# Kernel optimization log

Measured on AMD Instinct MI355X. Metric: run time of the kernel, lower is better.

Reference implementation:

```python
import jax, jax.numpy as jnp
import numpy as np

NUM_HEADS = 16

def _apply_rope(t, cos, sin):
    # t: [B, nh, S, hd]; cos/sin: [S, hd//2]
    t1 = t[..., 0::2]
    t2 = t[..., 1::2]
    c = cos[None, None, :, :]
    s = sin[None, None, :, :]
    r1 = t1 * c - t2 * s
    r2 = t1 * s + t2 * c
    # interleave back to [..., hd]
    out = jnp.stack([r1, r2], axis=-1)
    return out.reshape(t.shape)

def setup_inputs() -> dict:
    key = jax.random.key(0)
    ks = jax.random.split(key, 6)
    B, S, H = 1, 4096, 1024
    hd = H // NUM_HEADS
    x = jax.random.normal(ks[0], (B, S, H), dtype=jnp.float32)
    # RoPE angle matrix: theta[pos, i] = pos / 10000^(2i/hd), shape [context, hd//2]
    pos = jnp.arange(S, dtype=jnp.float32)[:, None]
    inv_freq = 1.0 / (10000.0 ** (jnp.arange(0, hd, 2, dtype=jnp.float32) / hd))
    rotation = pos * inv_freq[None, :]
    sc = 1.0 / np.sqrt(H)
    W_qkv = jax.random.normal(ks[1], (H, 3 * H), dtype=jnp.float32) * sc
    b_qkv = jax.random.normal(ks[2], (3 * H,), dtype=jnp.float32) * 0.01
    W_out = jax.random.normal(ks[3], (H, H), dtype=jnp.float32) * sc
    b_out = jax.random.normal(ks[4], (H,), dtype=jnp.float32) * 0.01
    return {"x": x, "rotation": rotation, "W_qkv": W_qkv, "b_qkv": b_qkv,
            "W_out": W_out, "b_out": b_out, "window_size": 33}

def reference(x, rotation, W_qkv, b_qkv, W_out, b_out, window_size):
    B, S, H = x.shape
    nh = NUM_HEADS
    hd = H // nh
    W = window_size
    pad = W // 2
    qkv = x @ W_qkv + b_qkv                               # [B, S, 3H]
    qkv = qkv.reshape(B, S, nh, 3 * hd).transpose(0, 2, 1, 3)  # [B, nh, S, 3hd]
    q, k, v = jnp.split(qkv, 3, axis=-1)                  # each [B, nh, S, hd]
    cos = jnp.cos(rotation[:S])
    sin = jnp.sin(rotation[:S])
    q = _apply_rope(q, cos, sin)
    k = _apply_rope(k, cos, sin)
    # zero-pad along sequence, then gather sliding windows
    k_pad = jnp.pad(k, ((0, 0), (0, 0), (pad, pad), (0, 0)))
    v_pad = jnp.pad(v, ((0, 0), (0, 0), (pad, pad), (0, 0)))
    idx = jnp.arange(S)[:, None] + jnp.arange(W)[None, :]  # [S, W]
    k_win = k_pad[:, :, idx, :]                            # [B, nh, S, W, hd]
    v_win = v_pad[:, :, idx, :]
    scores = jnp.einsum('bnsh,bnswh->bnsw', q, k_win) / np.sqrt(hd)
    attn = jax.nn.softmax(scores, axis=-1)
    ctx = jnp.einsum('bnsw,bnswh->bnsh', attn, v_win)      # [B, nh, S, hd]
    ctx = ctx.transpose(0, 2, 1, 3).reshape(B, S, H)
    return ctx @ W_out + b_out
```

## Files before the change

### kernel.cpp

```cpp
#include <hip/hip_runtime.h>
#include <hip/hip_bf16.h>

#define S_LEN 4096
#define NH 16
#define HD 64
#define WIN 33
#define PAD 16
#define QT 64
#define KROWS 96
#define KPITCH_U 36

typedef short short8 __attribute__((ext_vector_type(8)));
typedef float f32x4 __attribute__((ext_vector_type(4)));

__device__ __forceinline__ float bl(unsigned u){ return __uint_as_float(u << 16); }
__device__ __forceinline__ float bh(unsigned u){ return __uint_as_float(u & 0xffff0000u); }
__device__ __forceinline__ unsigned f2bfu(float f){
  unsigned u = __float_as_uint(f);
  return (u + 0x7fffu + ((u >> 16) & 1u)) >> 16;
}
__device__ __forceinline__ unsigned pack2(float a, float b){ return f2bfu(a) | (f2bfu(b) << 16); }

__device__ __forceinline__ void gload_lds16(const void* g, void* l){
  __builtin_amdgcn_global_load_lds(
      (const __attribute__((address_space(1))) void*)g,
      (__attribute__((address_space(3))) void*)l, 16, 0, 0);
}


__global__ __launch_bounds__(256) void prep_all(
    const float* __restrict__ rot, float2* __restrict__ csq,
    const float* __restrict__ x, __hip_bfloat16* __restrict__ xb,
    const float* __restrict__ Wq, __hip_bfloat16* __restrict__ Wt1,
    const float* __restrict__ Wo, __hip_bfloat16* __restrict__ Wt2)
{
  __shared__ float tile[32][33];
  const int b = blockIdx.x, tid = threadIdx.x;
  if (b < 512) {
    int t = b * 256 + tid;
    float v = rot[t], sv, cv;
    __sincosf(v, &sv, &cv);
    csq[t] = make_float2(cv, sv);
  } else if (b < 2560) {
    int t = (b - 512) * 256 + tid;
    const float4* p = (const float4*)x + (size_t)t * 2;
    float4 a = p[0], c = p[1];
    uint4 o;
    o.x = pack2(a.x, a.y); o.y = pack2(a.z, a.w);
    o.z = pack2(c.x, c.y); o.w = pack2(c.z, c.w);
    ((uint4*)xb)[t] = o;
  } else {
    const float* in; unsigned short* out; int R, C, bx, by;
    if (b < 5632) { int bb = b - 2560; in = Wq; out = (unsigned short*)Wt1; R = 1024; C = 3072; bx = bb % 96; by = bb / 96; }
    else          { int bb = b - 5632; in = Wo; out = (unsigned short*)Wt2; R = 1024; C = 1024; bx = bb % 32; by = bb / 32; }
    int c0 = bx * 32, r0 = by * 32;
    int tx = tid & 31, ty = tid >> 5;
    #pragma unroll
    for (int i = 0; i < 4; ++i) {
      int r = ty + i * 8;
      tile[r][tx] = in[(size_t)(r0 + r) * C + c0 + tx];
    }
    __syncthreads();
    #pragma unroll
    for (int i = 0; i < 4; ++i) {
      int cc = ty + i * 8;
      out[(size_t)(c0 + cc) * R + r0 + tx] = (unsigned short)f2bfu(tile[tx][cc]);
    }
  }
}


__global__ __launch_bounds__(256, 4) void gemm_qkv_rope(
    const __hip_bfloat16* __restrict__ A,
    const __hip_bfloat16* __restrict__ Bt,
    const float* __restrict__ bias,
    const float2* __restrict__ csq,
    unsigned short* __restrict__ Cout,
    int M, int N, int K)
{
  __shared__ unsigned int lA[128 * 64 / 2];
  __shared__ unsigned int lB[96 * 64 / 2];
  const int tid = threadIdx.x;
  const int wave = tid >> 6, lane = tid & 63;
  const int m0 = blockIdx.y * 128, n0 = blockIdx.x * 96;
  const int wm = (wave >> 1) * 64, wn = (wave & 1) * 48;
  const int l16 = lane >> 4, l15 = lane & 15;

  f32x4 acc[4][3];
  #pragma unroll
  for (int i = 0; i < 4; ++i)
    #pragma unroll
    for (int j = 0; j < 3; ++j) acc[i][j] = (f32x4){0.f, 0.f, 0.f, 0.f};

  const int nkt = K / 64;
  for (int kt = 0; kt < nkt; ++kt) {
    __syncthreads();
    #pragma unroll
    for (int it = 0; it < 4; ++it) {
      const int c = it * 256 + tid;
      const int r = c >> 3, s8 = c & 7;
      const int ss = s8 ^ (r & 7);
      gload_lds16(A + (size_t)(m0 + r) * K + kt * 64 + ss * 8, (char*)lA + c * 16);
    }
    #pragma unroll
    for (int it = 0; it < 3; ++it) {
      const int c = it * 256 + tid;
      const int r = c >> 3, s8 = c & 7;
      const int ss = s8 ^ (r & 7);
      gload_lds16(Bt + (size_t)(n0 + r) * K + kt * 64 + ss * 8, (char*)lB + c * 16);
    }
    __syncthreads();
    #pragma unroll
    for (int ks = 0; ks < 2; ++ks) {
      short8 af[4], bfr[3];
      #pragma unroll
      for (int mi = 0; mi < 4; ++mi) {
        const int r = wm + mi * 16 + l15;
        const int slot = (ks * 4 + l16) ^ (r & 7);
        uint4 u = *(const uint4*)((const char*)lA + r * 128 + slot * 16);
        af[mi] = __builtin_bit_cast(short8, u);
      }
      #pragma unroll
      for (int ni = 0; ni < 3; ++ni) {
        const int r = wn + ni * 16 + l15;
        const int slot = (ks * 4 + l16) ^ (r & 7);
        uint4 u = *(const uint4*)((const char*)lB + r * 128 + slot * 16);
        bfr[ni] = __builtin_bit_cast(short8, u);
      }
      #pragma unroll
      for (int mi = 0; mi < 4; ++mi)
        #pragma unroll
        for (int ni = 0; ni < 3; ++ni)
          acc[mi][ni] = __builtin_amdgcn_mfma_f32_16x16x32_bf16(af[mi], bfr[ni], acc[mi][ni], 0, 0, 0);
    }
  }

  #pragma unroll
  for (int ni = 0; ni < 3; ++ni) {
    const int cn = n0 + wn + ni * 16 + l15;
    const int rseg = cn % 192;
    const float bv = bias[cn];
    if (rseg < 128) {
      const int i = (rseg & 63) >> 1;
      const float sgn = (cn & 1) ? 1.f : -1.f;
      #pragma unroll
      for (int mi = 0; mi < 4; ++mi) {
        #pragma unroll
        for (int j = 0; j < 4; ++j) {
          const int rm = m0 + wm + mi * 16 + l16 * 4 + j;
          const float v = acc[mi][ni][j] + bv;
          const float p = __shfl_xor(v, 1);
          const float2 cs = csq[rm * 32 + i];
          Cout[(size_t)rm * N + cn] = (unsigned short)f2bfu(v * cs.x + p * (sgn * cs.y));
        }
      }
    } else {
      #pragma unroll
      for (int mi = 0; mi < 4; ++mi) {
        #pragma unroll
        for (int j = 0; j < 4; ++j) {
          const int rm = m0 + wm + mi * 16 + l16 * 4 + j;
          Cout[(size_t)rm * N + cn] = (unsigned short)f2bfu(acc[mi][ni][j] + bv);
        }
      }
    }
  }
}


__global__ __launch_bounds__(256, 4) void gemm_out64(
    const __hip_bfloat16* __restrict__ A,
    const __hip_bfloat16* __restrict__ Bt,
    const float* __restrict__ bias,
    float* __restrict__ Cout,
    int M, int N, int K)
{
  __shared__ unsigned int lA[2][64 * 64 / 2];
  __shared__ unsigned int lB[2][64 * 64 / 2];
  const int tid = threadIdx.x;
  const int wave = tid >> 6, lane = tid & 63;
  const int m0 = blockIdx.y * 64, n0 = blockIdx.x * 64;
  const int wm = (wave >> 1) * 32, wn = (wave & 1) * 32;
  const int l16 = lane >> 4, l15 = lane & 15;

  f32x4 acc[2][2];
  #pragma unroll
  for (int i = 0; i < 2; ++i)
    #pragma unroll
    for (int j = 0; j < 2; ++j) acc[i][j] = (f32x4){0.f, 0.f, 0.f, 0.f};

  auto stage = [&](int buf, int kt) {
    #pragma unroll
    for (int it = 0; it < 2; ++it) {
      const int c = it * 256 + tid;
      const int r = c >> 3, s8 = c & 7;
      const int ss = s8 ^ (r & 7);
      gload_lds16(A  + (size_t)(m0 + r) * K + kt * 64 + ss * 8, (char*)lA[buf] + c * 16);
      gload_lds16(Bt + (size_t)(n0 + r) * K + kt * 64 + ss * 8, (char*)lB[buf] + c * 16);
    }
  };

  const int nkt = K / 64;
  stage(0, 0);
  int cur = 0;
  for (int kt = 0; kt < nkt; ++kt) {
    const bool pf = (kt + 1 < nkt);
    if (pf) stage(cur ^ 1, kt + 1);
    if (pf) asm volatile("s_waitcnt vmcnt(4)" ::: "memory");
    else    asm volatile("s_waitcnt vmcnt(0)" ::: "memory");
    __builtin_amdgcn_s_barrier();
    __builtin_amdgcn_sched_barrier(0);
    #pragma unroll
    for (int ks = 0; ks < 2; ++ks) {
      short8 af[2], bfr[2];
      #pragma unroll
      for (int mi = 0; mi < 2; ++mi) {
        const int r = wm + mi * 16 + l15;
        const int slot = (ks * 4 + l16) ^ (r & 7);
        uint4 u = *(const uint4*)((const char*)lA[cur] + r * 128 + slot * 16);
        af[mi] = __builtin_bit_cast(short8, u);
      }
      #pragma unroll
      for (int ni = 0; ni < 2; ++ni) {
        const int r = wn + ni * 16 + l15;
        const int slot = (ks * 4 + l16) ^ (r & 7);
        uint4 u = *(const uint4*)((const char*)lB[cur] + r * 128 + slot * 16);
        bfr[ni] = __builtin_bit_cast(short8, u);
      }
      __builtin_amdgcn_s_setprio(1);
      #pragma unroll
      for (int mi = 0; mi < 2; ++mi)
        #pragma unroll
        for (int ni = 0; ni < 2; ++ni)
          acc[mi][ni] = __builtin_amdgcn_mfma_f32_16x16x32_bf16(af[mi], bfr[ni], acc[mi][ni], 0, 0, 0);
      __builtin_amdgcn_s_setprio(0);
    }
    __builtin_amdgcn_sched_barrier(0);
    __builtin_amdgcn_s_barrier();
    cur ^= 1;
  }

  #pragma unroll
  for (int ni = 0; ni < 2; ++ni) {
    const int cn = n0 + wn + ni * 16 + l15;
    const float bv = bias[cn];
    #pragma unroll
    for (int mi = 0; mi < 2; ++mi) {
      #pragma unroll
      for (int j = 0; j < 4; ++j) {
        const int rm = m0 + wm + mi * 16 + l16 * 4 + j;
        Cout[(size_t)rm * N + cn] = acc[mi][ni][j] + bv;
      }
    }
  }
}


__global__ __launch_bounds__(256) void attn_kernel(const __hip_bfloat16* __restrict__ qkv,
                                                   __hip_bfloat16* __restrict__ ctx){
  __shared__ unsigned int kbuf[KROWS * KPITCH_U];
  __shared__ unsigned int vbuf[KROWS * KPITCH_U];
  const int tid = threadIdx.x;
  const int h   = blockIdx.x & 15;
  const int qs0 = (blockIdx.x >> 4) * QT;

  #pragma unroll
  for (int it = 0; it < 3; ++it) {
    int c = tid + it * 256;
    int r = c >> 3, s8 = c & 7;
    int srow = qs0 - PAD + r;
    uint4 kv = make_uint4(0, 0, 0, 0), vv = make_uint4(0, 0, 0, 0);
    if ((unsigned)srow < (unsigned)S_LEN) {
      kv = ((const uint4*)(qkv + (size_t)srow * 3072 + h * 192 + 64))[s8];
      vv = ((const uint4*)(qkv + (size_t)srow * 3072 + h * 192 + 128))[s8];
    }
    *(uint4*)(kbuf + r * KPITCH_U + s8 * 4) = kv;
    *(uint4*)(vbuf + r * KPITCH_U + s8 * 4) = vv;
  }

  const int ql = tid >> 2, t4 = tid & 3;
  const uint4* qp = (const uint4*)(qkv + (size_t)(qs0 + ql) * 3072 + h * 192);
  float qf[64];
  #pragma unroll
  for (int c = 0; c < 8; ++c) {
    uint4 v = qp[c];
    qf[c*8+0] = bl(v.x); qf[c*8+1] = bh(v.x);
    qf[c*8+2] = bl(v.y); qf[c*8+3] = bh(v.y);
    qf[c*8+4] = bl(v.z); qf[c*8+5] = bh(v.z);
    qf[c*8+6] = bl(v.w); qf[c*8+7] = bh(v.w);
  }
  __syncthreads();

  float sc[9];
  #pragma unroll
  for (int j = 0; j < 9; ++j) sc[j] = 0.f;
  float mx = -1e30f;
  #pragma unroll
  for (int j = 0; j < 9; ++j) {
    int w = t4 + 4 * j;
    if (w < WIN) {
      int rw = ql + w;
      const uint4* kp = (const uint4*)(kbuf + rw * KPITCH_U);
      float d = 0.f;
      #pragma unroll
      for (int c = 0; c < 8; ++c) {
        uint4 kv = kp[c];
        d += qf[c*8+0]*bl(kv.x) + qf[c*8+1]*bh(kv.x)
           + qf[c*8+2]*bl(kv.y) + qf[c*8+3]*bh(kv.y)
           + qf[c*8+4]*bl(kv.z) + qf[c*8+5]*bh(kv.z)
           + qf[c*8+6]*bl(kv.w) + qf[c*8+7]*bh(kv.w);
      }
      sc[j] = d * 0.125f;
      mx = fmaxf(mx, sc[j]);
    }
  }
  mx = fmaxf(mx, __shfl_xor(mx, 1));
  mx = fmaxf(mx, __shfl_xor(mx, 2));
  float sum = 0.f;
  #pragma unroll
  for (int j = 0; j < 9; ++j) {
    int w = t4 + 4 * j;
    if (w < WIN) { sc[j] = __expf(sc[j] - mx); sum += sc[j]; }
  }
  sum += __shfl_xor(sum, 1);
  sum += __shfl_xor(sum, 2);
  const float inv = 1.0f / sum;
  #pragma unroll
  for (int j = 0; j < 9; ++j) sc[j] *= inv;

  float accd[16];
  #pragma unroll
  for (int i = 0; i < 16; ++i) accd[i] = 0.f;
  #pragma unroll
  for (int w = 0; w < WIN; ++w) {
    float wgt = __shfl(sc[w >> 2], ((tid & 63) & ~3) | (w & 3), 64);
    int rw = ql + w;
    const uint4* vp = (const uint4*)(vbuf + rw * KPITCH_U + t4 * 8);
    uint4 a = vp[0], b = vp[1];
    float vf[16];
    vf[0]=bl(a.x); vf[1]=bh(a.x); vf[2]=bl(a.y); vf[3]=bh(a.y);
    vf[4]=bl(a.z); vf[5]=bh(a.z); vf[6]=bl(a.w); vf[7]=bh(a.w);
    vf[8]=bl(b.x); vf[9]=bh(b.x); vf[10]=bl(b.y); vf[11]=bh(b.y);
    vf[12]=bl(b.z); vf[13]=bh(b.z); vf[14]=bl(b.w); vf[15]=bh(b.w);
    #pragma unroll
    for (int i = 0; i < 16; ++i) accd[i] += wgt * vf[i];
  }

  unsigned short* op = (unsigned short*)ctx + (size_t)(qs0 + ql) * 1024 + h * 64 + t4 * 16;
  uint4 o1, o2;
  o1.x = pack2(accd[0], accd[1]);  o1.y = pack2(accd[2], accd[3]);
  o1.z = pack2(accd[4], accd[5]);  o1.w = pack2(accd[6], accd[7]);
  o2.x = pack2(accd[8], accd[9]);  o2.y = pack2(accd[10], accd[11]);
  o2.z = pack2(accd[12], accd[13]); o2.w = pack2(accd[14], accd[15]);
  *(uint4*)op = o1;
  *((uint4*)op + 1) = o2;
}


extern "C" void kernel_launch(void* const* d_in, const int* in_sizes, int n_in,
                              void* d_out, int out_size, void* d_ws, size_t ws_size,
                              hipStream_t stream)
{
  const float* x     = (const float*)d_in[0];
  const float* rot   = (const float*)d_in[1];
  const float* W_qkv = (const float*)d_in[2];
  const float* b_qkv = (const float*)d_in[3];
  const float* W_out = (const float*)d_in[4];
  const float* b_out = (const float*)d_in[5];
  float* out = (float*)d_out;

  char* ws = (char*)d_ws;
  __hip_bfloat16* xb   = (__hip_bfloat16*)(ws + 0);
  __hip_bfloat16* Wt1  = (__hip_bfloat16*)(ws + 8388608);
  __hip_bfloat16* Wt2  = (__hip_bfloat16*)(ws + 14680064);
  __hip_bfloat16* qkvb = (__hip_bfloat16*)(ws + 16777216);
  __hip_bfloat16* ctx  = (__hip_bfloat16*)(ws + 41943040);
  float2* csq          = (float2*)(ws + 50331648);

  prep_all<<<6656, 256, 0, stream>>>(rot, csq, x, xb, W_qkv, Wt1, W_out, Wt2);
  gemm_qkv_rope<<<dim3(3072 / 96, 4096 / 128), 256, 0, stream>>>(xb, Wt1, b_qkv, csq,
                                                                 (unsigned short*)qkvb, 4096, 3072, 1024);
  attn_kernel<<<64 * 16, 256, 0, stream>>>(qkvb, ctx);
  gemm_out64<<<dim3(1024 / 64, 4096 / 64), 256, 0, stream>>>(ctx, Wt2, b_out, out, 4096, 1024, 1024);
}
```

Baseline: 87.33 us.

## Restructure QKV GEMM into 256x256 double-buffered tiles with 8 waves

The QKV+RoPE GEMM now uses 512-thread blocks computing 256x256 output tiles, with each wave owning a 128x64 sub-tile. Operand tiles are double-buffered in LDS (128 KB) and the next k-tile is prefetched while MFMAs run on the current one, using sched/s_barrier and setprio to interleave work. This aims to raise arithmetic intensity and hide global load latency. In exchange the grid shrinks to 192 blocks, fewer than the number of CUs, occupancy drops to one block per CU, and register pressure rises with 128 accumulator floats per thread.

Result: slower. 93.60 us (+7.2%).

```diff
diff --git a/kernel.cpp b/kernel.cpp
--- a/kernel.cpp
+++ b/kernel.cpp
@@ -70,7 +70,7 @@
 }
 
 
-__global__ __launch_bounds__(256, 4) void gemm_qkv_rope(
+__global__ __launch_bounds__(512) void gemm_qkv_rope(
     const __hip_bfloat16* __restrict__ A,
     const __hip_bfloat16* __restrict__ Bt,
     const float* __restrict__ bias,
@@ -78,77 +78,104 @@
     unsigned short* __restrict__ Cout,
     int M, int N, int K)
 {
-  __shared__ unsigned int lA[128 * 64 / 2];
-  __shared__ unsigned int lB[96 * 64 / 2];
+  __shared__ short lds[2][2][2][128][64];
   const int tid = threadIdx.x;
   const int wave = tid >> 6, lane = tid & 63;
-  const int m0 = blockIdx.y * 128, n0 = blockIdx.x * 96;
-  const int wm = (wave >> 1) * 64, wn = (wave & 1) * 48;
+  const int m0 = blockIdx.y * 256, n0 = blockIdx.x * 256;
+  const int wm = (wave >> 2) * 128, wn = (wave & 3) * 64;
   const int l16 = lane >> 4, l15 = lane & 15;
-
-  f32x4 acc[4][3];
-  #pragma unroll
-  for (int i = 0; i < 4; ++i)
-    #pragma unroll
-    for (int j = 0; j < 3; ++j) acc[i][j] = (f32x4){0.f, 0.f, 0.f, 0.f};
-
-  const int nkt = K / 64;
-  for (int kt = 0; kt < nkt; ++kt) {
-    __syncthreads();
-    #pragma unroll
-    for (int it = 0; it < 4; ++it) {
-      const int c = it * 256 + tid;
+  const int halfA = wave >> 2;
+  const int halfB = (wave >> 1) & 1;
+  const int rBbase = (wn & 64);
+
+  f32x4 acc[8][4];
+  #pragma unroll
+  for (int i = 0; i < 8; ++i)
+    #pragma unroll
+    for (int j = 0; j < 4; ++j) acc[i][j] = (f32x4){0.f, 0.f, 0.f, 0.f};
+
+  auto stage_ht = [&](int buf, int kt, int mat, int h) {
+    const __hip_bfloat16* src = mat ? Bt : A;
+    const int base = mat ? n0 : m0;
+    #pragma unroll
+    for (int it = 0; it < 2; ++it) {
+      const int c = it * 512 + tid;
       const int r = c >> 3, s8 = c & 7;
       const int ss = s8 ^ (r & 7);
-      gload_lds16(A + (size_t)(m0 + r) * K + kt * 64 + ss * 8, (char*)lA + c * 16);
-    }
-    #pragma unroll
-    for (int it = 0; it < 3; ++it) {
-      const int c = it * 256 + tid;
-      const int r = c >> 3, s8 = c & 7;
-      const int ss = s8 ^ (r & 7);
-      gload_lds16(Bt + (size_t)(n0 + r) * K + kt * 64 + ss * 8, (char*)lB + c * 16);
-    }
-    __syncthreads();
-    #pragma unroll
-    for (int ks = 0; ks < 2; ++ks) {
-      short8 af[4], bfr[3];
-      #pragma unroll
-      for (int mi = 0; mi < 4; ++mi) {
-        const int r = wm + mi * 16 + l15;
-        const int slot = (ks * 4 + l16) ^ (r & 7);
-        uint4 u = *(const uint4*)((const char*)lA + r * 128 + slot * 16);
-        af[mi] = __builtin_bit_cast(short8, u);
-      }
-      #pragma unroll
-      for (int ni = 0; ni < 3; ++ni) {
-        const int r = wn + ni * 16 + l15;
-        const int slot = (ks * 4 + l16) ^ (r & 7);
-        uint4 u = *(const uint4*)((const char*)lB + r * 128 + slot * 16);
-        bfr[ni] = __builtin_bit_cast(short8, u);
-      }
-      #pragma unroll
-      for (int mi = 0; mi < 4; ++mi)
-        #pragma unroll
-        for (int ni = 0; ni < 3; ++ni)
-          acc[mi][ni] = __builtin_amdgcn_mfma_f32_16x16x32_bf16(af[mi], bfr[ni], acc[mi][ni], 0, 0, 0);
-    }
-  }
-
-  #pragma unroll
-  for (int ni = 0; ni < 3; ++ni) {
-    const int cn = n0 + wn + ni * 16 + l15;
+      gload_lds16(src + (size_t)(base + h * 128 + r) * K + kt * 64 + ss * 8,
+                  (char*)&lds[buf][mat][h][0][0] + c * 16);
+    }
+  };
+  auto stage_tile = [&](int buf, int kt) {
+    stage_ht(buf, kt, 0, 0); stage_ht(buf, kt, 0, 1);
+    stage_ht(buf, kt, 1, 0); stage_ht(buf, kt, 1, 1);
+  };
+
+  const int nkt = K / 64;
+  stage_tile(0, 0);
+  asm volatile("s_waitcnt vmcnt(0)" ::: "memory");
+  __builtin_amdgcn_s_barrier();
+
+  for (int kt = 0; kt < nkt; ++kt) {
+    const int cur = kt & 1;
+    const bool pf = (kt + 1 < nkt);
+    short8 af[4][2];
+    #pragma unroll
+    for (int p = 0; p < 4; ++p) {
+      const int mh = p >> 1, nq = p & 1;
+      if (nq == 0) {
+        #pragma unroll
+        for (int mi = 0; mi < 4; ++mi)
+          #pragma unroll
+          for (int ks = 0; ks < 2; ++ks) {
+            const int r = mh * 64 + mi * 16 + l15;
+            const int slot = (ks * 4 + l16) ^ (r & 7);
+            af[mi][ks] = *(const short8*)&lds[cur][0][halfA][r][slot * 8];
+          }
+      }
+      short8 bf[2][2];
+      #pragma unroll
+      for (int ni = 0; ni < 2; ++ni)
+        #pragma unroll
+        for (int ks = 0; ks < 2; ++ks) {
+          const int r = rBbase + nq * 32 + ni * 16 + l15;
+          const int slot = (ks * 4 + l16) ^ (r & 7);
+          bf[ni][ks] = *(const short8*)&lds[cur][1][halfB][r][slot * 8];
+        }
+      if (p == 0 && pf) stage_tile(cur ^ 1, kt + 1);
+      __builtin_amdgcn_sched_barrier(0);
+      __builtin_amdgcn_s_barrier();
+      __builtin_amdgcn_s_setprio(1);
+      #pragma unroll
+      for (int ks = 0; ks < 2; ++ks)
+        #pragma unroll
+        for (int mi = 0; mi < 4; ++mi)
+          #pragma unroll
+          for (int ni = 0; ni < 2; ++ni)
+            acc[mh * 4 + mi][nq * 2 + ni] =
+                __builtin_amdgcn_mfma_f32_16x16x32_bf16(af[mi][ks], bf[ni][ks],
+                                                        acc[mh * 4 + mi][nq * 2 + ni], 0, 0, 0);
+      __builtin_amdgcn_s_setprio(0);
+      __builtin_amdgcn_sched_barrier(0);
+      if (p == 3 && pf) asm volatile("s_waitcnt vmcnt(0)" ::: "memory");
+      __builtin_amdgcn_s_barrier();
+    }
+  }
+
+  #pragma unroll
+  for (int bj = 0; bj < 4; ++bj) {
+    const int cn = n0 + wn + bj * 16 + l15;
     const int rseg = cn % 192;
     const float bv = bias[cn];
     if (rseg < 128) {
       const int i = (rseg & 63) >> 1;
       const float sgn = (cn & 1) ? 1.f : -1.f;
       #pragma unroll
-      for (int mi = 0; mi < 4; ++mi) {
+      for (int ai = 0; ai < 8; ++ai) {
         #pragma unroll
         for (int j = 0; j < 4; ++j) {
-          const int rm = m0 + wm + mi * 16 + l16 * 4 + j;
-          const float v = acc[mi][ni][j] + bv;
+          const int rm = m0 + wm + ai * 16 + l16 * 4 + j;
+          const float v = acc[ai][bj][j] + bv;
           const float p = __shfl_xor(v, 1);
           const float2 cs = csq[rm * 32 + i];
           Cout[(size_t)rm * N + cn] = (unsigned short)f2bfu(v * cs.x + p * (sgn * cs.y));
@@ -156,11 +183,11 @@
       }
     } else {
       #pragma unroll
-      for (int mi = 0; mi < 4; ++mi) {
+      for (int ai = 0; ai < 8; ++ai) {
         #pragma unroll
         for (int j = 0; j < 4; ++j) {
-          const int rm = m0 + wm + mi * 16 + l16 * 4 + j;
-          Cout[(size_t)rm * N + cn] = (unsigned short)f2bfu(acc[mi][ni][j] + bv);
+          const int rm = m0 + wm + ai * 16 + l16 * 4 + j;
+          Cout[(size_t)rm * N + cn] = (unsigned short)f2bfu(acc[ai][bj][j] + bv);
         }
       }
     }
@@ -378,8 +405,8 @@
   float2* csq          = (float2*)(ws + 50331648);
 
   prep_all<<<6656, 256, 0, stream>>>(rot, csq, x, xb, W_qkv, Wt1, W_out, Wt2);
-  gemm_qkv_rope<<<dim3(3072 / 96, 4096 / 128), 256, 0, stream>>>(xb, Wt1, b_qkv, csq,
-                                                                 (unsigned short*)qkvb, 4096, 3072, 1024);
+  gemm_qkv_rope<<<dim3(3072 / 256, 4096 / 256), 512, 0, stream>>>(xb, Wt1, b_qkv, csq,
+                                                                  (unsigned short*)qkvb, 4096, 3072, 1024);
   attn_kernel<<<64 * 16, 256, 0, stream>>>(qkvb, ctx);
   gemm_out64<<<dim3(1024 / 64, 4096 / 64), 256, 0, stream>>>(ctx, Wt2, b_out, out, 4096, 1024, 1024);
 }
```

## Enlarge QKV GEMM tile to 256x192 with double-buffered LDS prefetch

Applied to the files above, without the earlier changes.

The fused QKV+RoPE GEMM now uses 512-thread blocks computing 256x192 tiles, and the LDS buffers are double-buffered so the next K-tile's global->LDS loads overlap the current MFMA work. Synchronisation uses raw barriers plus explicit vmcnt waits. The larger tile is meant to raise data reuse and cut the number of blocks, and the prefetch is meant to hide load latency. In exchange there is a single large block per CU, which lowers occupancy and latency hiding, and the grid is only 256 blocks.

Result: slower. 90.19 us (+3.3%).

```diff
diff --git a/kernel.cpp b/kernel.cpp
--- a/kernel.cpp
+++ b/kernel.cpp
@@ -70,7 +70,7 @@
 }
 
 
-__global__ __launch_bounds__(256, 4) void gemm_qkv_rope(
+__global__ __launch_bounds__(512) void gemm_qkv_rope(
     const __hip_bfloat16* __restrict__ A,
     const __hip_bfloat16* __restrict__ Bt,
     const float* __restrict__ bias,
@@ -78,77 +78,85 @@
     unsigned short* __restrict__ Cout,
     int M, int N, int K)
 {
-  __shared__ unsigned int lA[128 * 64 / 2];
-  __shared__ unsigned int lB[96 * 64 / 2];
+  __shared__ short lA[2][256][64];
+  __shared__ short lB[2][192][64];
   const int tid = threadIdx.x;
   const int wave = tid >> 6, lane = tid & 63;
-  const int m0 = blockIdx.y * 128, n0 = blockIdx.x * 96;
-  const int wm = (wave >> 1) * 64, wn = (wave & 1) * 48;
+  const int m0 = blockIdx.y * 256, n0 = blockIdx.x * 192;
+  const int wm = (wave >> 2) * 128, wn = (wave & 3) * 48;
   const int l16 = lane >> 4, l15 = lane & 15;
 
-  f32x4 acc[4][3];
-  #pragma unroll
-  for (int i = 0; i < 4; ++i)
+  f32x4 acc[8][3];
+  #pragma unroll
+  for (int i = 0; i < 8; ++i)
     #pragma unroll
     for (int j = 0; j < 3; ++j) acc[i][j] = (f32x4){0.f, 0.f, 0.f, 0.f};
 
-  const int nkt = K / 64;
-  for (int kt = 0; kt < nkt; ++kt) {
-    __syncthreads();
+  auto stage = [&](int buf, int kt) {
     #pragma unroll
     for (int it = 0; it < 4; ++it) {
-      const int c = it * 256 + tid;
+      const int c = it * 512 + tid;
       const int r = c >> 3, s8 = c & 7;
       const int ss = s8 ^ (r & 7);
-      gload_lds16(A + (size_t)(m0 + r) * K + kt * 64 + ss * 8, (char*)lA + c * 16);
+      gload_lds16(A + (size_t)(m0 + r) * K + kt * 64 + ss * 8,
+                  (char*)&lA[buf][0][0] + c * 16);
     }
     #pragma unroll
     for (int it = 0; it < 3; ++it) {
-      const int c = it * 256 + tid;
+      const int c = it * 512 + tid;
       const int r = c >> 3, s8 = c & 7;
       const int ss = s8 ^ (r & 7);
-      gload_lds16(Bt + (size_t)(n0 + r) * K + kt * 64 + ss * 8, (char*)lB + c * 16);
-    }
-    __syncthreads();
+      gload_lds16(Bt + (size_t)(n0 + r) * K + kt * 64 + ss * 8,
+                  (char*)&lB[buf][0][0] + c * 16);
+    }
+  };
+
+  const int nkt = K / 64;
+  stage(0, 0);
+  for (int kt = 0; kt < nkt; ++kt) {
+    const int cur = kt & 1;
+    __builtin_amdgcn_s_barrier();
+    if (kt + 1 < nkt) stage(cur ^ 1, kt + 1);
+    if (kt + 1 < nkt) asm volatile("s_waitcnt vmcnt(7)" ::: "memory");
+    else              asm volatile("s_waitcnt vmcnt(0)" ::: "memory");
+    __builtin_amdgcn_s_barrier();
     #pragma unroll
     for (int ks = 0; ks < 2; ++ks) {
-      short8 af[4], bfr[3];
-      #pragma unroll
-      for (int mi = 0; mi < 4; ++mi) {
+      short8 af[8], bf[3];
+      #pragma unroll
+      for (int mi = 0; mi < 8; ++mi) {
         const int r = wm + mi * 16 + l15;
         const int slot = (ks * 4 + l16) ^ (r & 7);
-        uint4 u = *(const uint4*)((const char*)lA + r * 128 + slot * 16);
-        af[mi] = __builtin_bit_cast(short8, u);
+        af[mi] = *(const short8*)&lA[cur][r][slot * 8];
       }
       #pragma unroll
       for (int ni = 0; ni < 3; ++ni) {
         const int r = wn + ni * 16 + l15;
         const int slot = (ks * 4 + l16) ^ (r & 7);
-        uint4 u = *(const uint4*)((const char*)lB + r * 128 + slot * 16);
-        bfr[ni] = __builtin_bit_cast(short8, u);
-      }
-      #pragma unroll
-      for (int mi = 0; mi < 4; ++mi)
+        bf[ni] = *(const short8*)&lB[cur][r][slot * 8];
+      }
+      #pragma unroll
+      for (int mi = 0; mi < 8; ++mi)
         #pragma unroll
         for (int ni = 0; ni < 3; ++ni)
-          acc[mi][ni] = __builtin_amdgcn_mfma_f32_16x16x32_bf16(af[mi], bfr[ni], acc[mi][ni], 0, 0, 0);
-    }
-  }
-
-  #pragma unroll
-  for (int ni = 0; ni < 3; ++ni) {
-    const int cn = n0 + wn + ni * 16 + l15;
-    const int rseg = cn % 192;
+          acc[mi][ni] = __builtin_amdgcn_mfma_f32_16x16x32_bf16(af[mi], bf[ni], acc[mi][ni], 0, 0, 0);
+    }
+  }
+
+  #pragma unroll
+  for (int bj = 0; bj < 3; ++bj) {
+    const int cn = n0 + wn + bj * 16 + l15;
+    const int rseg = wn + bj * 16 + l15;
     const float bv = bias[cn];
     if (rseg < 128) {
       const int i = (rseg & 63) >> 1;
       const float sgn = (cn & 1) ? 1.f : -1.f;
       #pragma unroll
-      for (int mi = 0; mi < 4; ++mi) {
+      for (int ai = 0; ai < 8; ++ai) {
         #pragma unroll
         for (int j = 0; j < 4; ++j) {
-          const int rm = m0 + wm + mi * 16 + l16 * 4 + j;
-          const float v = acc[mi][ni][j] + bv;
+          const int rm = m0 + wm + ai * 16 + l16 * 4 + j;
+          const float v = acc[ai][bj][j] + bv;
           const float p = __shfl_xor(v, 1);
           const float2 cs = csq[rm * 32 + i];
           Cout[(size_t)rm * N + cn] = (unsigned short)f2bfu(v * cs.x + p * (sgn * cs.y));
@@ -156,11 +164,11 @@
       }
     } else {
       #pragma unroll
-      for (int mi = 0; mi < 4; ++mi) {
+      for (int ai = 0; ai < 8; ++ai) {
         #pragma unroll
         for (int j = 0; j < 4; ++j) {
-          const int rm = m0 + wm + mi * 16 + l16 * 4 + j;
-          Cout[(size_t)rm * N + cn] = (unsigned short)f2bfu(acc[mi][ni][j] + bv);
+          const int rm = m0 + wm + ai * 16 + l16 * 4 + j;
+          Cout[(size_t)rm * N + cn] = (unsigned short)f2bfu(acc[ai][bj][j] + bv);
         }
       }
     }
@@ -378,8 +386,8 @@
   float2* csq          = (float2*)(ws + 50331648);
 
   prep_all<<<6656, 256, 0, stream>>>(rot, csq, x, xb, W_qkv, Wt1, W_out, Wt2);
-  gemm_qkv_rope<<<dim3(3072 / 96, 4096 / 128), 256, 0, stream>>>(xb, Wt1, b_qkv, csq,
-                                                                 (unsigned short*)qkvb, 4096, 3072, 1024);
+  gemm_qkv_rope<<<dim3(3072 / 192, 4096 / 256), 512, 0, stream>>>(xb, Wt1, b_qkv, csq,
+                                                                  (unsigned short*)qkvb, 4096, 3072, 1024);
   attn_kernel<<<64 * 16, 256, 0, stream>>>(qkvb, ctx);
   gemm_out64<<<dim3(1024 / 64, 4096 / 64), 256, 0, stream>>>(ctx, Wt2, b_out, out, 4096, 1024, 1024);
 }
```
